# Kernel tuning notes

Measured on AMD Instinct MI355X. Metric: run time of the kernel, lower is better.

The kernel has to match this reference:

```python
import jax, jax.numpy as jnp
import numpy as np

N = 4096      # nodes
F = 128       # input feature dim
HEADS = 8     # attention_num
U = 8         # units per head


def setup_inputs() -> dict:
    key = jax.random.key(0)
    k_a, k_h, k_w, k_al, k_ar = jax.random.split(key, 5)
    A = jax.random.randint(k_a, (N, N), 0, 2).astype(jnp.float32)   # dense 0/1 adjacency
    H = jax.random.normal(k_h, (N, F), dtype=jnp.float32)
    W = jax.random.normal(k_w, (HEADS, F, U), dtype=jnp.float32) * 0.1
    a_left = jax.random.normal(k_al, (HEADS, U), dtype=jnp.float32) * 0.1
    a_right = jax.random.normal(k_ar, (HEADS, U), dtype=jnp.float32) * 0.1
    return {"A": A, "H": H, "W": W, "a_left": a_left, "a_right": a_right}


def reference(A, H, W, a_left, a_right):
    # Per-head attention logits: E[h,i,j] = e_left[h,i] + e_right[h,j]
    e_l = jnp.einsum('nf,hfu,hu->hn', H, W, a_left)    # [HEADS, N]
    e_r = jnp.einsum('nf,hfu,hu->hn', H, W, a_right)   # [HEADS, N]
    E = e_l[:, :, None] + e_r[:, None, :]              # [HEADS, N, N]
    # Faithful to original: denominator uses exp(E * A) (zeros in A -> exp(0)=1)
    denom = jnp.sum(jnp.exp(E * A[None]), axis=-1, keepdims=True)   # [HEADS, N, 1]
    Alpha = jnp.exp(E) / denom * A[None]               # masked attention weights
    # Aggregate then project: elu(Alpha @ H @ W) per head
    out = jax.nn.elu(jnp.einsum('hij,jf,hfu->hiu', Alpha, H, W))    # [HEADS, N, U]
    # is_output_layer=False -> concat heads along feature dim: [N, HEADS*U]
    return jnp.transpose(out, (1, 0, 2)).reshape(H.shape[0], HEADS * U)
```

## Files before the change

### kernel.cpp

```cpp
#include <hip/hip_runtime.h>
#include <hip/hip_bf16.h>

#define NN 4096
#define FF 128
#define NC 80
#define LSTR 84

typedef __attribute__((ext_vector_type(4))) float float4v;
typedef __attribute__((ext_vector_type(4))) unsigned int uint4v;
typedef __attribute__((ext_vector_type(8))) short short8;

static __device__ inline unsigned short bfb(float x) {
    __hip_bfloat16 b = __float2bfloat16(x);
    return *(unsigned short*)&b;
}
static __device__ inline float bff(unsigned short u) {
    __hip_bfloat16 b = *(__hip_bfloat16*)&u;
    return __bfloat162float(b);
}
static __device__ inline uint4v ntload(const unsigned int* p) {
    return __builtin_nontemporal_load((const uint4v*)p);
}

__global__ __launch_bounds__(640) void gat_wsplit(const float* __restrict__ W,
                                                  const float* __restrict__ al,
                                                  const float* __restrict__ ar,
                                                  __hip_bfloat16* __restrict__ Wphi,
                                                  __hip_bfloat16* __restrict__ Wplo)
{
    const int c  = threadIdx.x;
    const int f0 = threadIdx.y * 16;
    float av[8];
    const int hc = (c - 64) & 7;
    if (c >= 64) {
        const float* ap = (c < 72) ? ar : al;
        #pragma unroll
        for (int u = 0; u < 8; ++u) av[u] = ap[hc * 8 + u];
    }
    #pragma unroll
    for (int i = 0; i < 16; ++i) {
        const int f = f0 + i;
        float val;
        if (c < 64) {
            val = W[(size_t)(c >> 3) * (FF * 8) + (size_t)f * 8 + (c & 7)];
        } else {
            const float* wp = W + (size_t)hc * (FF * 8) + (size_t)f * 8;
            float s = 0.f;
            #pragma unroll
            for (int u = 0; u < 8; ++u) s += wp[u] * av[u];
            val = s;
        }
        const unsigned short h = bfb(val);
        const unsigned short l = bfb(val - bff(h));
        const int g = (f >> 5) * 4 + ((f >> 3) & 3);
        const size_t idx = ((size_t)g * NC + c) * 8 + (f & 7);
        Wphi[idx] = *(const __hip_bfloat16*)&h;
        Wplo[idx] = *(const __hip_bfloat16*)&l;
    }
}

__global__ __launch_bounds__(64) void gat_prep(const float* __restrict__ H,
                                               const __hip_bfloat16* __restrict__ Wphi,
                                               const __hip_bfloat16* __restrict__ Wplo,
                                               float* __restrict__ expEl,
                                               __hip_bfloat16* __restrict__ Bp)
{
    const int lane = threadIdx.x;
    const int j0 = blockIdx.x * 16;
    const int m16 = lane & 15, q = lane >> 4;
    const short* Whs = (const short*)Wphi;
    const short* Wls = (const short*)Wplo;

    float4v acc[5] = {};
    #pragma unroll
    for (int kt = 0; kt < 4; ++kt) {
        const float* hp = H + (size_t)(j0 + m16) * FF + kt * 32 + q * 8;
        float4v x0 = *(const float4v*)hp;
        float4v x1 = *(const float4v*)(hp + 4);
        short8 ahi, alo;
        #pragma unroll
        for (int i = 0; i < 4; ++i) {
            const unsigned short h0 = bfb(x0[i]);
            ahi[i] = (short)h0;
            alo[i] = (short)bfb(x0[i] - bff(h0));
            const unsigned short h1 = bfb(x1[i]);
            ahi[4 + i] = (short)h1;
            alo[4 + i] = (short)bfb(x1[i] - bff(h1));
        }
        const short8* bh = (const short8*)(Whs + (size_t)(kt * 4 + q) * NC * 8);
        const short8* bl = (const short8*)(Wls + (size_t)(kt * 4 + q) * NC * 8);
        #pragma unroll
        for (int nt = 0; nt < 5; ++nt) {
            short8 bhi = bh[nt * 16 + m16];
            short8 blo = bl[nt * 16 + m16];
            acc[nt] = __builtin_amdgcn_mfma_f32_16x16x32_bf16(ahi, bhi, acc[nt], 0, 0, 0);
            acc[nt] = __builtin_amdgcn_mfma_f32_16x16x32_bf16(alo, bhi, acc[nt], 0, 0, 0);
            acc[nt] = __builtin_amdgcn_mfma_f32_16x16x32_bf16(ahi, blo, acc[nt], 0, 0, 0);
        }
    }

    const int jbase = j0 + q * 4;
    float ex[4];
    #pragma unroll
    for (int r = 0; r < 4; ++r) ex[r] = expf(acc[4][r]);
    if (m16 >= 8) {
        #pragma unroll
        for (int r = 0; r < 4; ++r)
            expEl[(m16 - 8) * NN + jbase + r] = ex[r];
    }
    #pragma unroll
    for (int r = 0; r < 4; ++r) {
        const int j = jbase + r;
        const size_t base = ((size_t)((j >> 5) * 4 + ((j >> 3) & 3)) * NC) * 8 + (j & 7);
        #pragma unroll
        for (int nt = 0; nt < 4; ++nt) {
            const int srcl = (lane & 48) | (nt * 2 + (m16 >> 3));
            const float er = __shfl(ex[r], srcl);
            Bp[base + (size_t)(nt * 16 + m16) * 8] = __float2bfloat16(er * acc[nt][r]);
        }
        const float v = (m16 < 8) ? ex[r] : (m16 == 8 ? 1.0f : 0.0f);
        Bp[base + (size_t)(64 + m16) * 8] = __float2bfloat16(v);
    }
}

__global__ __launch_bounds__(1024) void gat_gemm(const float* __restrict__ A,
                                                 const __hip_bfloat16* __restrict__ Bp,
                                                 const float* __restrict__ expEl,
                                                 float* __restrict__ out)
{
    __shared__ float Ls[16 * 16 * LSTR];
    const int rb   = blockIdx.x;
    const int wave = threadIdx.x >> 6;
    const int lane = threadIdx.x & 63;
    const int m16  = lane & 15;
    const int q    = lane >> 4;
    const int row0 = rb * 16;

    float4v acc[5] = {};

    const int k0 = wave * 256;
    const unsigned int* Au = (const unsigned int*)A;
    const short* Bs = (const short*)Bp;
    const unsigned int* arow = Au + (size_t)(row0 + m16) * NN + q * 8 + k0;

    uint4v a0[2], a1[2];
    a0[0] = ntload(arow);      a1[0] = ntload(arow + 4);
    a0[1] = ntload(arow + 32); a1[1] = ntload(arow + 36);

    #pragma unroll
    for (int kt = 0; kt < 8; ++kt) {
        const int cur = kt & 1;
        short8 afrag;
        afrag[0] = (short)(a0[cur][0] >> 16); afrag[1] = (short)(a0[cur][1] >> 16);
        afrag[2] = (short)(a0[cur][2] >> 16); afrag[3] = (short)(a0[cur][3] >> 16);
        afrag[4] = (short)(a1[cur][0] >> 16); afrag[5] = (short)(a1[cur][1] >> 16);
        afrag[6] = (short)(a1[cur][2] >> 16); afrag[7] = (short)(a1[cur][3] >> 16);

        if (kt + 2 < 8) {
            a0[cur] = ntload(arow + (kt + 2) * 32);
            a1[cur] = ntload(arow + (kt + 2) * 32 + 4);
        }

        const int ktg = wave * 8 + kt;
        const short8* bbase = (const short8*)(Bs + ((size_t)(ktg * 4 + q) * NC) * 8);
        #pragma unroll
        for (int nt = 0; nt < 5; ++nt) {
            short8 bfrag = bbase[nt * 16 + m16];
            acc[nt] = __builtin_amdgcn_mfma_f32_16x16x32_bf16(afrag, bfrag, acc[nt], 0, 0, 0);
        }
    }

    float* Lw = Ls + wave * (16 * LSTR);
    #pragma unroll
    for (int nt = 0; nt < 5; ++nt) {
        #pragma unroll
        for (int r = 0; r < 4; ++r)
            Lw[(q * 4 + r) * LSTR + nt * 16 + m16] = acc[nt][r];
    }
    __syncthreads();

    {
        const int p  = threadIdx.x;
        const int il = p >> 6;
        const int c  = p & 63;
        const int h  = c >> 3;
        float T = 0.f, S = 0.f, dg = 0.f;
        #pragma unroll
        for (int w = 0; w < 16; ++w) {
            const float* rowp = Ls + w * (16 * LSTR) + il * LSTR;
            T  += rowp[c];
            S  += rowp[64 + h];
            dg += rowp[72];
        }
        const float el = expEl[h * NN + row0 + il];
        const float denom = ((float)NN - dg) + el * S;
        const float x = el * T / denom;
        out[(size_t)(row0 + il) * 64 + c] = x > 0.f ? x : expf(x) - 1.f;
    }
}

extern "C" void kernel_launch(void* const* d_in, const int* in_sizes, int n_in,
                              void* d_out, int out_size, void* d_ws, size_t ws_size,
                              hipStream_t stream) {
    const float* A  = (const float*)d_in[0];
    const float* H  = (const float*)d_in[1];
    const float* W  = (const float*)d_in[2];
    const float* al = (const float*)d_in[3];
    const float* ar = (const float*)d_in[4];
    float* out = (float*)d_out;

    float* expEl = (float*)d_ws;
    __hip_bfloat16* Bp   = (__hip_bfloat16*)((char*)d_ws + 131072);
    __hip_bfloat16* Wphi = (__hip_bfloat16*)((char*)d_ws + 131072 + 655360);
    __hip_bfloat16* Wplo = (__hip_bfloat16*)((char*)d_ws + 131072 + 655360 + 20480);

    gat_wsplit<<<1, dim3(80, 8), 0, stream>>>(W, al, ar, Wphi, Wplo);
    gat_prep<<<NN / 16, 64, 0, stream>>>(H, Wphi, Wplo, expEl, Bp);
    gat_gemm<<<NN / 16, 1024, 0, stream>>>(A, Bp, expEl, out);
}
```

Before: 132.9 us.

## Halve GEMM block size, drop nontemporal prefetch, parallelize weight split

The weight-split kernel now runs as 40 blocks with one element per thread instead of a single block looping. The main GEMM uses 8 waves per block, each covering twice the K range, with a single-stage regular load prefetch in place of the two-deep nontemporal prefetch. The reduction loops over 8 partials, with each thread handling two outputs. This lowers per-block LDS and thread count but reduces in-flight memory requests per row block.

After: 119.8 us. 9.9% less time.

```diff
diff --git a/kernel.cpp b/kernel.cpp
--- a/kernel.cpp
+++ b/kernel.cpp
@@ -18,52 +18,42 @@
     __hip_bfloat16 b = *(__hip_bfloat16*)&u;
     return __bfloat162float(b);
 }
-static __device__ inline uint4v ntload(const unsigned int* p) {
-    return __builtin_nontemporal_load((const uint4v*)p);
-}
-
-__global__ __launch_bounds__(640) void gat_wsplit(const float* __restrict__ W,
+
+__global__ __launch_bounds__(256) void gat_wsplit(const float* __restrict__ W,
                                                   const float* __restrict__ al,
                                                   const float* __restrict__ ar,
                                                   __hip_bfloat16* __restrict__ Wphi,
                                                   __hip_bfloat16* __restrict__ Wplo)
 {
-    const int c  = threadIdx.x;
-    const int f0 = threadIdx.y * 16;
-    float av[8];
-    const int hc = (c - 64) & 7;
-    if (c >= 64) {
+    const int tid = blockIdx.x * 256 + threadIdx.x;
+    if (tid >= 80 * FF) return;
+    const int c = tid % 80;
+    const int f = tid / 80;
+    float val;
+    if (c < 64) {
+        val = W[(size_t)(c >> 3) * (FF * 8) + (size_t)f * 8 + (c & 7)];
+    } else {
+        const int hc = (c - 64) & 7;
         const float* ap = (c < 72) ? ar : al;
-        #pragma unroll
-        for (int u = 0; u < 8; ++u) av[u] = ap[hc * 8 + u];
-    }
-    #pragma unroll
-    for (int i = 0; i < 16; ++i) {
-        const int f = f0 + i;
-        float val;
-        if (c < 64) {
-            val = W[(size_t)(c >> 3) * (FF * 8) + (size_t)f * 8 + (c & 7)];
-        } else {
-            const float* wp = W + (size_t)hc * (FF * 8) + (size_t)f * 8;
-            float s = 0.f;
-            #pragma unroll
-            for (int u = 0; u < 8; ++u) s += wp[u] * av[u];
-            val = s;
-        }
-        const unsigned short h = bfb(val);
-        const unsigned short l = bfb(val - bff(h));
-        const int g = (f >> 5) * 4 + ((f >> 3) & 3);
-        const size_t idx = ((size_t)g * NC + c) * 8 + (f & 7);
-        Wphi[idx] = *(const __hip_bfloat16*)&h;
-        Wplo[idx] = *(const __hip_bfloat16*)&l;
-    }
-}
-
-__global__ __launch_bounds__(64) void gat_prep(const float* __restrict__ H,
-                                               const __hip_bfloat16* __restrict__ Wphi,
-                                               const __hip_bfloat16* __restrict__ Wplo,
-                                               float* __restrict__ expEl,
-                                               __hip_bfloat16* __restrict__ Bp)
+        const float* wp = W + (size_t)hc * (FF * 8) + (size_t)f * 8;
+        float s = 0.f;
+        #pragma unroll
+        for (int u = 0; u < 8; ++u) s += wp[u] * ap[hc * 8 + u];
+        val = s;
+    }
+    const unsigned short h = bfb(val);
+    const unsigned short l = bfb(val - bff(h));
+    const int g = (f >> 5) * 4 + ((f >> 3) & 3);
+    const size_t idx = ((size_t)g * NC + c) * 8 + (f & 7);
+    Wphi[idx] = *(const __hip_bfloat16*)&h;
+    Wplo[idx] = *(const __hip_bfloat16*)&l;
+}
+
+__global__ __launch_bounds__(64, 1) void gat_prep(const float* __restrict__ H,
+                                                  const __hip_bfloat16* __restrict__ Wphi,
+                                                  const __hip_bfloat16* __restrict__ Wplo,
+                                                  float* __restrict__ expEl,
+                                                  __hip_bfloat16* __restrict__ Bp)
 {
     const int lane = threadIdx.x;
     const int j0 = blockIdx.x * 16;
@@ -123,12 +113,12 @@
     }
 }
 
-__global__ __launch_bounds__(1024) void gat_gemm(const float* __restrict__ A,
-                                                 const __hip_bfloat16* __restrict__ Bp,
-                                                 const float* __restrict__ expEl,
-                                                 float* __restrict__ out)
+__global__ __launch_bounds__(512) void gat_gemm(const float* __restrict__ A,
+                                                const __hip_bfloat16* __restrict__ Bp,
+                                                const float* __restrict__ expEl,
+                                                float* __restrict__ out)
 {
-    __shared__ float Ls[16 * 16 * LSTR];
+    __shared__ float Ls[8 * 16 * LSTR];
     const int rb   = blockIdx.x;
     const int wave = threadIdx.x >> 6;
     const int lane = threadIdx.x & 63;
@@ -138,30 +128,29 @@
 
     float4v acc[5] = {};
 
-    const int k0 = wave * 256;
+    const int k0 = wave * 512;
     const unsigned int* Au = (const unsigned int*)A;
     const short* Bs = (const short*)Bp;
-    const unsigned int* arow = Au + (size_t)(row0 + m16) * NN + q * 8 + k0;
-
-    uint4v a0[2], a1[2];
-    a0[0] = ntload(arow);      a1[0] = ntload(arow + 4);
-    a0[1] = ntload(arow + 32); a1[1] = ntload(arow + 36);
-
-    #pragma unroll
-    for (int kt = 0; kt < 8; ++kt) {
-        const int cur = kt & 1;
+    const unsigned int* arow = Au + (size_t)(row0 + m16) * NN + q * 8;
+
+    uint4v a0 = *(const uint4v*)(arow + k0);
+    uint4v a1 = *(const uint4v*)(arow + k0 + 4);
+
+    #pragma unroll 4
+    for (int kt = 0; kt < 16; ++kt) {
+        const int kk = k0 + kt * 32;
         short8 afrag;
-        afrag[0] = (short)(a0[cur][0] >> 16); afrag[1] = (short)(a0[cur][1] >> 16);
-        afrag[2] = (short)(a0[cur][2] >> 16); afrag[3] = (short)(a0[cur][3] >> 16);
-        afrag[4] = (short)(a1[cur][0] >> 16); afrag[5] = (short)(a1[cur][1] >> 16);
-        afrag[6] = (short)(a1[cur][2] >> 16); afrag[7] = (short)(a1[cur][3] >> 16);
-
-        if (kt + 2 < 8) {
-            a0[cur] = ntload(arow + (kt + 2) * 32);
-            a1[cur] = ntload(arow + (kt + 2) * 32 + 4);
-        }
-
-        const int ktg = wave * 8 + kt;
+        afrag[0] = (short)(a0[0] >> 16); afrag[1] = (short)(a0[1] >> 16);
+        afrag[2] = (short)(a0[2] >> 16); afrag[3] = (short)(a0[3] >> 16);
+        afrag[4] = (short)(a1[0] >> 16); afrag[5] = (short)(a1[1] >> 16);
+        afrag[6] = (short)(a1[2] >> 16); afrag[7] = (short)(a1[3] >> 16);
+
+        if (kt + 1 < 16) {
+            a0 = *(const uint4v*)(arow + kk + 32);
+            a1 = *(const uint4v*)(arow + kk + 36);
+        }
+
+        const int ktg = kk >> 5;
         const short8* bbase = (const short8*)(Bs + ((size_t)(ktg * 4 + q) * NC) * 8);
         #pragma unroll
         for (int nt = 0; nt < 5; ++nt) {
@@ -179,14 +168,14 @@
     }
     __syncthreads();
 
-    {
-        const int p  = threadIdx.x;
+    #pragma unroll
+    for (int p = threadIdx.x; p < 1024; p += 512) {
         const int il = p >> 6;
         const int c  = p & 63;
         const int h  = c >> 3;
         float T = 0.f, S = 0.f, dg = 0.f;
         #pragma unroll
-        for (int w = 0; w < 16; ++w) {
+        for (int w = 0; w < 8; ++w) {
             const float* rowp = Ls + w * (16 * LSTR) + il * LSTR;
             T  += rowp[c];
             S  += rowp[64 + h];
@@ -214,7 +203,7 @@
     __hip_bfloat16* Wphi = (__hip_bfloat16*)((char*)d_ws + 131072 + 655360);
     __hip_bfloat16* Wplo = (__hip_bfloat16*)((char*)d_ws + 131072 + 655360 + 20480);
 
-    gat_wsplit<<<1, dim3(80, 8), 0, stream>>>(W, al, ar, Wphi, Wplo);
+    gat_wsplit<<<40, 256, 0, stream>>>(W, al, ar, Wphi, Wplo);
     gat_prep<<<NN / 16, 64, 0, stream>>>(H, Wphi, Wplo, expEl, Bp);
-    gat_gemm<<<NN / 16, 1024, 0, stream>>>(A, Bp, expEl, out);
-}
+    gat_gemm<<<NN / 16, 512, 0, stream>>>(A, Bp, expEl, out);
+}
```
